# Kernel optimization log

Measured on AMD Instinct MI355X. Metric: run time of the kernel, lower is better.

Reference implementation:

```python
import jax, jax.numpy as jnp
import numpy as np

HASH_BUCKETS = 1024
D_MODEL = 256


def setup_inputs() -> dict:
    key = jax.random.key(0)
    ks = jax.random.split(key, 12)
    batch_a, batch_b, n_keys, d = 4096, 8192, 4, D_MODEL
    inp = {
        "table_a_emb": jax.random.normal(ks[0], (batch_a, d), dtype=jnp.float32),
        "table_b_emb": jax.random.normal(ks[1], (batch_b, d), dtype=jnp.float32),
        "keys_a": jax.random.randint(ks[2], (batch_a, n_keys), 0, 1000000, dtype=jnp.int64) if jax.config.jax_enable_x64 else jax.random.randint(ks[2], (batch_a, n_keys), 0, 1000000, dtype=jnp.int32),
        "keys_b": jax.random.randint(ks[3], (batch_b, n_keys), 0, 1000000, dtype=jnp.int64) if jax.config.jax_enable_x64 else jax.random.randint(ks[3], (batch_b, n_keys), 0, 1000000, dtype=jnp.int32),
        # SimpleMLP(d_in=2d, d_hidden=2d, n_hidden=1, d_out=d): in->hidden ReLU, hidden->out
        "W1": jax.random.normal(ks[4], (2 * d, 2 * d), dtype=jnp.float32) * (1.0 / np.sqrt(2 * d)),
        "b1": jnp.zeros((2 * d,), dtype=jnp.float32),
        "W2": jax.random.normal(ks[5], (2 * d, d), dtype=jnp.float32) * (1.0 / np.sqrt(2 * d)),
        "b2": jnp.zeros((d,), dtype=jnp.float32),
        "Wo": jax.random.normal(ks[6], (d, d), dtype=jnp.float32) * (1.0 / np.sqrt(d)),
        "bo": jnp.zeros((d,), dtype=jnp.float32),
    }
    return inp


def reference(table_a_emb, table_b_emb, keys_a, keys_b, W1, b1, W2, b2, Wo, bo):
    # hash-bucket matching: row i of table_a matches all rows of table_b with equal hash
    hash_a = jnp.sum(keys_a, axis=1) % HASH_BUCKETS  # (batch_a,)
    hash_b = jnp.sum(keys_b, axis=1) % HASH_BUCKETS  # (batch_b,)
    mask = (hash_a[:, None] == hash_b[None, :]).astype(table_b_emb.dtype)  # (batch_a, batch_b)
    count = mask.sum(axis=1, keepdims=True)  # (batch_a, 1)
    # mean of matched table_b embeddings; zeros when no match (matches torch loop semantics)
    agg_b = (mask @ table_b_emb) / jnp.maximum(count, 1.0)  # (batch_a, d)
    combined = jnp.concatenate([table_a_emb, agg_b], axis=-1)  # (batch_a, 2d)
    h = jax.nn.relu(combined @ W1 + b1)
    rel = h @ W2 + b2
    return rel @ Wo + bo
```

## Files before the change

### kernel.cpp

```cpp
#include <hip/hip_runtime.h>
#include <hip/hip_bf16.h>

#define HASH_BUCKETS 1024
#define BA 4096
#define BB 8192

typedef __attribute__((ext_vector_type(8))) short bf16x8;
typedef __attribute__((ext_vector_type(4))) float f32x4;

__device__ __forceinline__ short f2bf(float x) {
    union { float f; unsigned int u; } c;
    c.f = x;
    unsigned int lsb = (c.u >> 16) & 1u;
    c.u += 0x7fffu + lsb;
    return (short)(c.u >> 16);
}

__device__ __forceinline__ void gl_lds16(const void* g, void* l) {
    __builtin_amdgcn_global_load_lds((const __attribute__((address_space(1))) void*)g,
                                     (__attribute__((address_space(3))) void*)l, 16, 0, 0);
}

template <int MODE>
__device__ __forceinline__ void gemm_tile(short* __restrict__ As, short* __restrict__ Bs,
                                          const short* __restrict__ A,
                                          const short* __restrict__ Bt,
                                          const short* __restrict__ tab,
                                          const short* __restrict__ bmean,
                                          const int* __restrict__ ha,
                                          const float* __restrict__ bias,
                                          void* __restrict__ Cv,
                                          int bm, int bn, int M, int N, int K) {
    const int tid = threadIdx.x;
    const int l = tid & 63, w = tid >> 6;
    const int wm = w >> 1, wn = w & 1;

    const int sr = w * 4 + (l >> 4);
    const int sk = ((l & 15) ^ (sr & 7)) * 8;
    int harr[4];
    if (MODE == 0) {
#pragma unroll
        for (int c = 0; c < 4; ++c) harr[c] = ha[bm + c * 16 + sr];
    }
    const int lr = l & 15;
    const int g = l >> 4;
    f32x4 acc[2][2] = {};

    auto STAGE = [&](int nb, int kt) {
        const int k0 = kt * 128;
#pragma unroll
        for (int c = 0; c < 4; ++c) {
            const int r = c * 16 + sr;
            const short* asrc;
            if (MODE == 0) {
                asrc = (k0 < 256) ? &tab[(size_t)(bm + r) * 256 + k0 + sk]
                                  : &bmean[(size_t)harr[c] * 256 + (k0 - 256) + sk];
            } else {
                asrc = &A[(size_t)(bm + r) * K + k0 + sk];
            }
            gl_lds16(asrc, As + nb * 8192 + (c * 16 + w * 4) * 128);
            gl_lds16(&Bt[(size_t)(bn + r) * K + k0 + sk],
                     Bs + nb * 8192 + (c * 16 + w * 4) * 128);
        }
    };

    auto COMPUTE = [&](int nb) {
        const short* ab = As + nb * 8192;
        const short* bb = Bs + nb * 8192;
        bf16x8 af[2][4], bfr[2][4];
#pragma unroll
        for (int mf = 0; mf < 2; ++mf) {
            const int rr = wm * 32 + mf * 16 + lr;
#pragma unroll
            for (int ks = 0; ks < 4; ++ks)
                af[mf][ks] = *(const bf16x8*)&ab[rr * 128 + (((ks * 4 + g) ^ (rr & 7)) * 8)];
        }
#pragma unroll
        for (int nf = 0; nf < 2; ++nf) {
            const int rr = wn * 32 + nf * 16 + lr;
#pragma unroll
            for (int ks = 0; ks < 4; ++ks)
                bfr[nf][ks] = *(const bf16x8*)&bb[rr * 128 + (((ks * 4 + g) ^ (rr & 7)) * 8)];
        }
#pragma unroll
        for (int ks = 0; ks < 4; ++ks)
#pragma unroll
            for (int mf = 0; mf < 2; ++mf)
#pragma unroll
                for (int nf = 0; nf < 2; ++nf)
                    acc[mf][nf] = __builtin_amdgcn_mfma_f32_16x16x32_bf16(
                        af[mf][ks], bfr[nf][ks], acc[mf][nf], 0, 0, 0);
    };

    const int nt = K >> 7;
    STAGE(0, 0);
    asm volatile("s_waitcnt vmcnt(0)" ::: "memory");
    __syncthreads();
    for (int t = 0; t < nt; ++t) {
        const int cur = t & 1;
        if (t + 1 < nt) STAGE(cur ^ 1, t + 1);
        COMPUTE(cur);
        asm volatile("s_waitcnt vmcnt(0)" ::: "memory");
        __syncthreads();
    }

#pragma unroll
    for (int mf = 0; mf < 2; ++mf)
#pragma unroll
        for (int nf = 0; nf < 2; ++nf) {
            const int col = bn + wn * 32 + nf * 16 + lr;
            const int rbase = bm + wm * 32 + mf * 16 + ((l >> 4) << 2);
            float bv = 0.f;
            if (MODE < 2) bv = bias[col];
#pragma unroll
            for (int i = 0; i < 4; ++i) {
                const float x = acc[mf][nf][i] + bv;
                const int row = rbase + i;
                if (MODE == 0)
                    ((short*)Cv)[(size_t)row * N + col] = f2bf(fmaxf(x, 0.f));
                else if (MODE == 1)
                    ((float*)Cv)[(size_t)row * N + col] = x;
                else
                    ((short*)Cv)[(size_t)col * M + row] = f2bf(x);
            }
        }
}

__device__ __forceinline__ void prep_job(int b, int t, char* smem,
                                         const float* W1, const float* Wo,
                                         const float* W2, const float* b2,
                                         const float* bo, const float* ta,
                                         const int* ka, short* W1T, short* WoT,
                                         short* W2b, short* tab, int* ha,
                                         float* bfused) {
    if (b < 64) {
        float(*tl)[65] = (float(*)[65])smem;
        const int tr = (b >> 3) * 64, tc = (b & 7) * 64;
        const int c = t & 63, r0 = t >> 6;
#pragma unroll
        for (int i = 0; i < 16; ++i) {
            int r = r0 + i * 4;
            tl[r][c] = W1[(size_t)(tr + r) * 512 + tc + c];
        }
        __syncthreads();
#pragma unroll
        for (int i = 0; i < 16; ++i) {
            int r = r0 + i * 4;
            W1T[(size_t)(tc + r) * 512 + tr + c] = f2bf(tl[c][r]);
        }
    } else if (b < 80) {
        float(*tl)[65] = (float(*)[65])smem;
        const int bb2 = b - 64;
        const int tr = (bb2 >> 2) * 64, tc = (bb2 & 3) * 64;
        const int c = t & 63, r0 = t >> 6;
#pragma unroll
        for (int i = 0; i < 16; ++i) {
            int r = r0 + i * 4;
            tl[r][c] = Wo[(size_t)(tr + r) * 256 + tc + c];
        }
        __syncthreads();
#pragma unroll
        for (int i = 0; i < 16; ++i) {
            int r = r0 + i * 4;
            WoT[(size_t)(tc + r) * 256 + tr + c] = f2bf(tl[c][r]);
        }
    } else if (b < 88) {
        const int g = (b - 80) * 256 + t;
#pragma unroll
        for (int i = 0; i < 16; ++i) {
            int e = g + i * 2048;
            float4 v = ((const float4*)W2)[e];
            short4 s;
            s.x = f2bf(v.x); s.y = f2bf(v.y); s.z = f2bf(v.z); s.w = f2bf(v.w);
            ((short4*)W2b)[e] = s;
        }
    } else if (b < 152) {
        const int bb2 = b - 88;
#pragma unroll
        for (int i = 0; i < 16; ++i) {
            int e = bb2 * 4096 + i * 256 + t;
            float4 v = ((const float4*)ta)[e];
            short4 s;
            s.x = f2bf(v.x); s.y = f2bf(v.y); s.z = f2bf(v.z); s.w = f2bf(v.w);
            ((short4*)tab)[e] = s;
        }
    } else if (b < 168) {
        const int r = (b - 152) * 256 + t;
        int4 k4 = ((const int4*)ka)[r];
        ha[r] = (k4.x + k4.y + k4.z + k4.w) & (HASH_BUCKETS - 1);
    } else if (b == 168) {
        float acc = bo[t];
        for (int k = 0; k < 256; ++k) acc += b2[k] * Wo[(size_t)k * 256 + t];
        bfused[t] = acc;
    }
}

__global__ __launch_bounds__(256) void prep_kernel(
    const float* __restrict__ W1, const float* __restrict__ Wo,
    const float* __restrict__ W2, const float* __restrict__ b2,
    const float* __restrict__ bo, const float* __restrict__ ta,
    const float* __restrict__ tb, const int* __restrict__ ka,
    const int* __restrict__ kb, short* __restrict__ W1T,
    short* __restrict__ WoT, short* __restrict__ W2b,
    short* __restrict__ tab, int* __restrict__ ha,
    float* __restrict__ bfused, short* __restrict__ bmean) {
    __shared__ __align__(16) char smem[16704];
    const int b = blockIdx.x;
    const int t = threadIdx.x;
    {
        float* part = (float*)smem;
        int* pcnt = (int*)(smem + 8192);
        const int h0 = 2 * b, h1 = 2 * b + 1;
        const int w = t >> 6, l = t & 63;
        float a0 = 0.f, a1 = 0.f, a2 = 0.f, a3 = 0.f;
        float c0f = 0.f, c1f = 0.f, c2f = 0.f, c3f = 0.f;
        int cnt0 = 0, cnt1 = 0;
        for (int it = 0; it < 32; ++it) {
            const int base = w * 2048 + it * 64;
            int4 k4 = ((const int4*)kb)[base + l];
            const int hh = (k4.x + k4.y + k4.z + k4.w) & 1023;
            unsigned long long m0 = __ballot(hh == h0);
            unsigned long long m1 = __ballot(hh == h1);
            cnt0 += __popcll(m0);
            cnt1 += __popcll(m1);
            while (m0) {
                int j = base + (__ffsll((long long)m0) - 1);
                m0 &= m0 - 1;
                const float* rp = tb + (size_t)j * 256;
                a0 += rp[l]; a1 += rp[l + 64]; a2 += rp[l + 128]; a3 += rp[l + 192];
            }
            while (m1) {
                int j = base + (__ffsll((long long)m1) - 1);
                m1 &= m1 - 1;
                const float* rp = tb + (size_t)j * 256;
                c0f += rp[l]; c1f += rp[l + 64]; c2f += rp[l + 128]; c3f += rp[l + 192];
            }
        }
        part[w * 256 + l] = a0; part[w * 256 + l + 64] = a1;
        part[w * 256 + l + 128] = a2; part[w * 256 + l + 192] = a3;
        part[1024 + w * 256 + l] = c0f; part[1024 + w * 256 + l + 64] = c1f;
        part[1024 + w * 256 + l + 128] = c2f; part[1024 + w * 256 + l + 192] = c3f;
        if (l == 0) { pcnt[w] = cnt0; pcnt[4 + w] = cnt1; }
        __syncthreads();
        float s0 = part[t] + part[256 + t] + part[512 + t] + part[768 + t];
        float s1 = part[1024 + t] + part[1280 + t] + part[1536 + t] + part[1792 + t];
        int n0 = pcnt[0] + pcnt[1] + pcnt[2] + pcnt[3];
        int n1 = pcnt[4] + pcnt[5] + pcnt[6] + pcnt[7];
        bmean[(size_t)h0 * 256 + t] = f2bf(s0 / (float)max(n0, 1));
        bmean[(size_t)h1 * 256 + t] = f2bf(s1 / (float)max(n1, 1));
        __syncthreads();
    }
    prep_job(b, t, smem, W1, Wo, W2, b2, bo, ta, ka, W1T, WoT, W2b, tab, ha, bfused);
}

__global__ __launch_bounds__(256) void g1_kernel(const short* __restrict__ W1T,
                                                 const short* __restrict__ tab,
                                                 const short* __restrict__ bmean,
                                                 const int* __restrict__ ha,
                                                 const float* __restrict__ b1,
                                                 short* __restrict__ hbuf,
                                                 const short* __restrict__ W2b,
                                                 const short* __restrict__ WoT,
                                                 short* __restrict__ w2woT) {
    __shared__ short As[2 * 8192];
    __shared__ short Bs[2 * 8192];
    if (blockIdx.y < 64)
        gemm_tile<0>(As, Bs, nullptr, W1T, tab, bmean, ha, b1, hbuf,
                     blockIdx.y * 64, blockIdx.x * 64, BA, 512, 512);
    else
        gemm_tile<2>(As, Bs, W2b, WoT, nullptr, nullptr, nullptr, nullptr, w2woT,
                     blockIdx.x * 64, (blockIdx.y - 64) * 64, 512, 256, 256);
}

__global__ __launch_bounds__(256) void g2_kernel(const short* __restrict__ hbuf,
                                                 const short* __restrict__ w2woT,
                                                 const float* __restrict__ bfused,
                                                 float* __restrict__ out) {
    __shared__ short As[2 * 8192];
    __shared__ short Bs[2 * 8192];
    gemm_tile<1>(As, Bs, hbuf, w2woT, nullptr, nullptr, nullptr, bfused, out,
                 blockIdx.y * 64, blockIdx.x * 64, BA, 256, 512);
}

extern "C" void kernel_launch(void* const* d_in, const int* in_sizes, int n_in,
                              void* d_out, int out_size, void* d_ws, size_t ws_size,
                              hipStream_t stream) {
    const float* ta = (const float*)d_in[0];
    const float* tb = (const float*)d_in[1];
    const int* ka = (const int*)d_in[2];
    const int* kb = (const int*)d_in[3];
    const float* W1 = (const float*)d_in[4];
    const float* b1 = (const float*)d_in[5];
    const float* W2 = (const float*)d_in[6];
    const float* b2 = (const float*)d_in[7];
    const float* Wo = (const float*)d_in[8];
    const float* bo = (const float*)d_in[9];
    float* out = (float*)d_out;

    char* ws = (char*)d_ws;
    int* ha = (int*)(ws + 0);
    short* bmean = (short*)(ws + 16384);
    short* tab = (short*)(ws + 540672);
    short* W1T = (short*)(ws + 2637824);
    short* w2woT = (short*)(ws + 3162112);
    float* bfused = (float*)(ws + 3424256);
    short* hbuf = (short*)(ws + 3425280);
    short* WoT = (short*)(ws + 7619584);
    short* W2b = (short*)(ws + 7750656);

    prep_kernel<<<512, 256, 0, stream>>>(W1, Wo, W2, b2, bo, ta, tb, ka, kb,
                                         W1T, WoT, W2b, tab, ha, bfused, bmean);
    g1_kernel<<<dim3(8, 68), 256, 0, stream>>>(W1T, tab, bmean, ha, b1, hbuf,
                                               W2b, WoT, w2woT);
    g2_kernel<<<dim3(4, 64), 256, 0, stream>>>(hbuf, w2woT, bfused, out);
}
```

Baseline: 40.39 us.

## Halve GEMM K-tile to 64 and split prep jobs into separate blocks

The GEMM tile's K step drops from 128 to 64. This halves LDS per buffer (from 64KB to 32KB per block), which may let more blocks share a CU. The staging and swizzle indexing are rewritten for 64-wide rows. The prep kernel now runs the weight and hash preparation jobs in their own 169 blocks instead of appending them to the bucket-mean blocks, so the grid grows to 681 and the serial tail per block shortens. The cost is twice as many K iterations and barriers in each GEMM tile.

```diff
diff --git a/kernel.cpp b/kernel.cpp
--- a/kernel.cpp
+++ b/kernel.cpp
@@ -35,55 +35,62 @@
     const int l = tid & 63, w = tid >> 6;
     const int wm = w >> 1, wn = w & 1;
 
-    const int sr = w * 4 + (l >> 4);
-    const int sk = ((l & 15) ^ (sr & 7)) * 8;
-    int harr[4];
-    if (MODE == 0) {
-#pragma unroll
-        for (int c = 0; c < 4; ++c) harr[c] = ha[bm + c * 16 + sr];
-    }
+    const int r0 = (w * 2 + 0) * 8 + (l >> 3);
+    const int r1 = (w * 2 + 1) * 8 + (l >> 3);
+    const int sk0 = ((l & 7) ^ (r0 & 7)) * 8;
+    const int sk1 = ((l & 7) ^ (r1 & 7)) * 8;
+    const int arow0 = bm + r0, arow1 = bm + r1;
+    const int brow0 = bn + r0, brow1 = bn + r1;
+    int ha0 = 0, ha1 = 0;
+    if (MODE == 0) { ha0 = ha[arow0]; ha1 = ha[arow1]; }
+    const int dst0 = (w * 2 + 0) * 512;
+    const int dst1 = (w * 2 + 1) * 512;
+
     const int lr = l & 15;
     const int g = l >> 4;
     f32x4 acc[2][2] = {};
 
     auto STAGE = [&](int nb, int kt) {
-        const int k0 = kt * 128;
-#pragma unroll
-        for (int c = 0; c < 4; ++c) {
-            const int r = c * 16 + sr;
-            const short* asrc;
-            if (MODE == 0) {
-                asrc = (k0 < 256) ? &tab[(size_t)(bm + r) * 256 + k0 + sk]
-                                  : &bmean[(size_t)harr[c] * 256 + (k0 - 256) + sk];
+        const int k0 = kt * 64;
+        const short *as0, *as1;
+        if (MODE == 0) {
+            if (k0 < 256) {
+                as0 = &tab[(size_t)arow0 * 256 + k0 + sk0];
+                as1 = &tab[(size_t)arow1 * 256 + k0 + sk1];
             } else {
-                asrc = &A[(size_t)(bm + r) * K + k0 + sk];
+                as0 = &bmean[(size_t)ha0 * 256 + (k0 - 256) + sk0];
+                as1 = &bmean[(size_t)ha1 * 256 + (k0 - 256) + sk1];
             }
-            gl_lds16(asrc, As + nb * 8192 + (c * 16 + w * 4) * 128);
-            gl_lds16(&Bt[(size_t)(bn + r) * K + k0 + sk],
-                     Bs + nb * 8192 + (c * 16 + w * 4) * 128);
-        }
+        } else {
+            as0 = &A[(size_t)arow0 * K + k0 + sk0];
+            as1 = &A[(size_t)arow1 * K + k0 + sk1];
+        }
+        gl_lds16(as0, As + nb * 4096 + dst0);
+        gl_lds16(as1, As + nb * 4096 + dst1);
+        gl_lds16(&Bt[(size_t)brow0 * K + k0 + sk0], Bs + nb * 4096 + dst0);
+        gl_lds16(&Bt[(size_t)brow1 * K + k0 + sk1], Bs + nb * 4096 + dst1);
     };
 
     auto COMPUTE = [&](int nb) {
-        const short* ab = As + nb * 8192;
-        const short* bb = Bs + nb * 8192;
-        bf16x8 af[2][4], bfr[2][4];
+        const short* ab = As + nb * 4096;
+        const short* bb = Bs + nb * 4096;
+        bf16x8 af[2][2], bfr[2][2];
 #pragma unroll
         for (int mf = 0; mf < 2; ++mf) {
             const int rr = wm * 32 + mf * 16 + lr;
 #pragma unroll
-            for (int ks = 0; ks < 4; ++ks)
-                af[mf][ks] = *(const bf16x8*)&ab[rr * 128 + (((ks * 4 + g) ^ (rr & 7)) * 8)];
+            for (int ks = 0; ks < 2; ++ks)
+                af[mf][ks] = *(const bf16x8*)&ab[rr * 64 + (((ks * 4 + g) ^ (lr & 7)) * 8)];
         }
 #pragma unroll
         for (int nf = 0; nf < 2; ++nf) {
             const int rr = wn * 32 + nf * 16 + lr;
 #pragma unroll
-            for (int ks = 0; ks < 4; ++ks)
-                bfr[nf][ks] = *(const bf16x8*)&bb[rr * 128 + (((ks * 4 + g) ^ (rr & 7)) * 8)];
-        }
-#pragma unroll
-        for (int ks = 0; ks < 4; ++ks)
+            for (int ks = 0; ks < 2; ++ks)
+                bfr[nf][ks] = *(const bf16x8*)&bb[rr * 64 + (((ks * 4 + g) ^ (lr & 7)) * 8)];
+        }
+#pragma unroll
+        for (int ks = 0; ks < 2; ++ks)
 #pragma unroll
             for (int mf = 0; mf < 2; ++mf)
 #pragma unroll
@@ -92,7 +99,7 @@
                         af[mf][ks], bfr[nf][ks], acc[mf][nf], 0, 0, 0);
     };
 
-    const int nt = K >> 7;
+    const int nt = K >> 6;
     STAGE(0, 0);
     asm volatile("s_waitcnt vmcnt(0)" ::: "memory");
     __syncthreads();
@@ -205,52 +212,53 @@
     short* __restrict__ tab, int* __restrict__ ha,
     float* __restrict__ bfused, short* __restrict__ bmean) {
     __shared__ __align__(16) char smem[16704];
-    const int b = blockIdx.x;
+    const int blk = blockIdx.x;
     const int t = threadIdx.x;
-    {
-        float* part = (float*)smem;
-        int* pcnt = (int*)(smem + 8192);
-        const int h0 = 2 * b, h1 = 2 * b + 1;
-        const int w = t >> 6, l = t & 63;
-        float a0 = 0.f, a1 = 0.f, a2 = 0.f, a3 = 0.f;
-        float c0f = 0.f, c1f = 0.f, c2f = 0.f, c3f = 0.f;
-        int cnt0 = 0, cnt1 = 0;
-        for (int it = 0; it < 32; ++it) {
-            const int base = w * 2048 + it * 64;
-            int4 k4 = ((const int4*)kb)[base + l];
-            const int hh = (k4.x + k4.y + k4.z + k4.w) & 1023;
-            unsigned long long m0 = __ballot(hh == h0);
-            unsigned long long m1 = __ballot(hh == h1);
-            cnt0 += __popcll(m0);
-            cnt1 += __popcll(m1);
-            while (m0) {
-                int j = base + (__ffsll((long long)m0) - 1);
-                m0 &= m0 - 1;
-                const float* rp = tb + (size_t)j * 256;
-                a0 += rp[l]; a1 += rp[l + 64]; a2 += rp[l + 128]; a3 += rp[l + 192];
-            }
-            while (m1) {
-                int j = base + (__ffsll((long long)m1) - 1);
-                m1 &= m1 - 1;
-                const float* rp = tb + (size_t)j * 256;
-                c0f += rp[l]; c1f += rp[l + 64]; c2f += rp[l + 128]; c3f += rp[l + 192];
-            }
-        }
-        part[w * 256 + l] = a0; part[w * 256 + l + 64] = a1;
-        part[w * 256 + l + 128] = a2; part[w * 256 + l + 192] = a3;
-        part[1024 + w * 256 + l] = c0f; part[1024 + w * 256 + l + 64] = c1f;
-        part[1024 + w * 256 + l + 128] = c2f; part[1024 + w * 256 + l + 192] = c3f;
-        if (l == 0) { pcnt[w] = cnt0; pcnt[4 + w] = cnt1; }
-        __syncthreads();
-        float s0 = part[t] + part[256 + t] + part[512 + t] + part[768 + t];
-        float s1 = part[1024 + t] + part[1280 + t] + part[1536 + t] + part[1792 + t];
-        int n0 = pcnt[0] + pcnt[1] + pcnt[2] + pcnt[3];
-        int n1 = pcnt[4] + pcnt[5] + pcnt[6] + pcnt[7];
-        bmean[(size_t)h0 * 256 + t] = f2bf(s0 / (float)max(n0, 1));
-        bmean[(size_t)h1 * 256 + t] = f2bf(s1 / (float)max(n1, 1));
-        __syncthreads();
+    if (blk < 169) {
+        prep_job(blk, t, smem, W1, Wo, W2, b2, bo, ta, ka, W1T, WoT, W2b, tab, ha, bfused);
+        return;
     }
-    prep_job(b, t, smem, W1, Wo, W2, b2, bo, ta, ka, W1T, WoT, W2b, tab, ha, bfused);
+    const int b = blk - 169;
+    float* part = (float*)smem;
+    int* pcnt = (int*)(smem + 8192);
+    const int h0 = 2 * b, h1 = 2 * b + 1;
+    const int w = t >> 6, l = t & 63;
+    float a0 = 0.f, a1 = 0.f, a2 = 0.f, a3 = 0.f;
+    float c0f = 0.f, c1f = 0.f, c2f = 0.f, c3f = 0.f;
+    int cnt0 = 0, cnt1 = 0;
+    for (int it = 0; it < 32; ++it) {
+        const int base = w * 2048 + it * 64;
+        int4 k4 = ((const int4*)kb)[base + l];
+        const int hh = (k4.x + k4.y + k4.z + k4.w) & 1023;
+        unsigned long long m0 = __ballot(hh == h0);
+        unsigned long long m1 = __ballot(hh == h1);
+        cnt0 += __popcll(m0);
+        cnt1 += __popcll(m1);
+        while (m0) {
+            int j = base + (__ffsll((long long)m0) - 1);
+            m0 &= m0 - 1;
+            const float* rp = tb + (size_t)j * 256;
+            a0 += rp[l]; a1 += rp[l + 64]; a2 += rp[l + 128]; a3 += rp[l + 192];
+        }
+        while (m1) {
+            int j = base + (__ffsll((long long)m1) - 1);
+            m1 &= m1 - 1;
+            const float* rp = tb + (size_t)j * 256;
+            c0f += rp[l]; c1f += rp[l + 64]; c2f += rp[l + 128]; c3f += rp[l + 192];
+        }
+    }
+    part[w * 256 + l] = a0; part[w * 256 + l + 64] = a1;
+    part[w * 256 + l + 128] = a2; part[w * 256 + l + 192] = a3;
+    part[1024 + w * 256 + l] = c0f; part[1024 + w * 256 + l + 64] = c1f;
+    part[1024 + w * 256 + l + 128] = c2f; part[1024 + w * 256 + l + 192] = c3f;
+    if (l == 0) { pcnt[w] = cnt0; pcnt[4 + w] = cnt1; }
+    __syncthreads();
+    float s0 = part[t] + part[256 + t] + part[512 + t] + part[768 + t];
+    float s1 = part[1024 + t] + part[1280 + t] + part[1536 + t] + part[1792 + t];
+    int n0 = pcnt[0] + pcnt[1] + pcnt[2] + pcnt[3];
+    int n1 = pcnt[4] + pcnt[5] + pcnt[6] + pcnt[7];
+    bmean[(size_t)h0 * 256 + t] = f2bf(s0 / (float)max(n0, 1));
+    bmean[(size_t)h1 * 256 + t] = f2bf(s1 / (float)max(n1, 1));
 }
 
 __global__ __launch_bounds__(256) void g1_kernel(const short* __restrict__ W1T,
@@ -262,8 +270,8 @@
                                                  const short* __restrict__ W2b,
                                                  const short* __restrict__ WoT,
                                                  short* __restrict__ w2woT) {
-    __shared__ short As[2 * 8192];
-    __shared__ short Bs[2 * 8192];
+    __shared__ short As[2 * 4096];
+    __shared__ short Bs[2 * 4096];
     if (blockIdx.y < 64)
         gemm_tile<0>(As, Bs, nullptr, W1T, tab, bmean, ha, b1, hbuf,
                      blockIdx.y * 64, blockIdx.x * 64, BA, 512, 512);
@@ -276,8 +284,8 @@
                                                  const short* __restrict__ w2woT,
                                                  const float* __restrict__ bfused,
                                                  float* __restrict__ out) {
-    __shared__ short As[2 * 8192];
-    __shared__ short Bs[2 * 8192];
+    __shared__ short As[2 * 4096];
+    __shared__ short Bs[2 * 4096];
     gemm_tile<1>(As, Bs, hbuf, w2woT, nullptr, nullptr, nullptr, bfused, out,
                  blockIdx.y * 64, blockIdx.x * 64, BA, 256, 512);
 }
@@ -308,7 +316,7 @@
     short* WoT = (short*)(ws + 7619584);
     short* W2b = (short*)(ws + 7750656);
 
-    prep_kernel<<<512, 256, 0, stream>>>(W1, Wo, W2, b2, bo, ta, tb, ka, kb,
+    prep_kernel<<<681, 256, 0, stream>>>(W1, Wo, W2, b2, bo, ta, tb, ka, kb,
                                          W1T, WoT, W2b, tab, ha, bfused, bmean);
     g1_kernel<<<dim3(8, 68), 256, 0, stream>>>(W1T, tab, bmean, ha, b1, hbuf,
                                                W2b, WoT, w2woT);
```

New measurement: 36.42 us. 1.11x faster.
